# Kernel optimization log

Measured on AMD Instinct MI355X. Metric: run time of the kernel, lower is better.

## Reference

```python
import jax, jax.numpy as jnp
import numpy as np

N = 4096
IN_DIM = 6
HID = 32
HEADS1 = 4
OUT_DIM = 64


def _gat_layer(x, mask, W, a_src, a_dst, b):
    # x: [n, in], W: [in, heads*d], a_src/a_dst: [heads, d], b: [heads*d]
    n = x.shape[0]
    heads, d = a_src.shape
    h = (x @ W).reshape(n, heads, d)                      # [n, heads, d]
    e_src = jnp.einsum('nhd,hd->nh', h, a_src)            # [n, heads]
    e_dst = jnp.einsum('nhd,hd->nh', h, a_dst)            # [n, heads]
    logits = e_src[:, None, :] + e_dst[None, :, :]        # [n, n, heads]
    logits = jax.nn.leaky_relu(logits, negative_slope=0.2)
    logits = jnp.where(mask[:, :, None], logits, jnp.float32(-1e9))
    alpha = jax.nn.softmax(logits, axis=1)                # softmax over j (dim=1)
    # dropout disabled (eval mode reference)
    out = jnp.einsum('ijh,jhd->ihd', alpha, h).reshape(n, heads * d)
    return out + b


def setup_inputs() -> dict:
    key = jax.random.key(0)
    ks = jax.random.split(key, 10)
    x = jax.random.normal(ks[0], (N, IN_DIM), dtype=jnp.float32)
    adj = jax.random.bernoulli(ks[1], 0.01, (N, N)).astype(jnp.float32)
    s = 0.1
    W1 = jax.random.normal(ks[2], (IN_DIM, HEADS1 * HID), dtype=jnp.float32) * s
    a_src1 = jax.random.normal(ks[3], (HEADS1, HID), dtype=jnp.float32) * s
    a_dst1 = jax.random.normal(ks[4], (HEADS1, HID), dtype=jnp.float32) * s
    b1 = jnp.zeros((HEADS1 * HID,), dtype=jnp.float32)
    W2 = jax.random.normal(ks[5], (HEADS1 * HID, OUT_DIM), dtype=jnp.float32) * s
    a_src2 = jax.random.normal(ks[6], (1, OUT_DIM), dtype=jnp.float32) * s
    a_dst2 = jax.random.normal(ks[7], (1, OUT_DIM), dtype=jnp.float32) * s
    b2 = jnp.zeros((OUT_DIM,), dtype=jnp.float32)
    return {'x': x, 'adj': adj, 'W1': W1, 'a_src1': a_src1, 'a_dst1': a_dst1,
            'b1': b1, 'W2': W2, 'a_src2': a_src2, 'a_dst2': a_dst2, 'b2': b2}


def reference(x, adj, W1, a_src1, a_dst1, b1, W2, a_src2, a_dst2, b2):
    n = x.shape[0]
    # add self loops: a = max(a, I), mask = a > 0
    a = jnp.maximum(adj, jnp.eye(n, dtype=adj.dtype))
    mask = a > 0
    h1 = jax.nn.elu(_gat_layer(x, mask, W1, a_src1, a_dst1, b1))
    # dropout disabled (eval mode)
    h2 = _gat_layer(h1, mask, W2, a_src2, a_dst2, b2)
    return h2
```

## Files before the change

kernel.cpp:

```cpp
#include <hip/hip_runtime.h>

#define N 4096
#define IN_DIM 6
#define HID 32
#define HEADS1 4
#define D1 (HEADS1*HID)
#define OUT_DIM 64
#define MAXNB 192

__global__ void kA(const float* __restrict__ x,
                   const float* __restrict__ W1,
                   const float* __restrict__ a_src1,
                   const float* __restrict__ a_dst1,
                   float* __restrict__ hpre,
                   float* __restrict__ es1,
                   float* __restrict__ ed1) {
    int t  = threadIdx.x;
    int r  = t >> 7;
    int tt = t & 127;
    int i  = blockIdx.x * 2 + r;
    __shared__ float xs[2][IN_DIM];
    if (tt < IN_DIM) xs[r][tt] = x[i*IN_DIM + tt];
    __syncthreads();
    float acc = 0.f;
    #pragma unroll
    for (int k = 0; k < IN_DIM; ++k)
        acc += xs[r][k] * W1[k*D1 + tt];
    hpre[(size_t)i*D1 + tt] = acc;
    float ps = acc * a_src1[tt];
    float pd = acc * a_dst1[tt];
    #pragma unroll
    for (int off = 16; off >= 1; off >>= 1) {
        ps += __shfl_xor(ps, off, 64);
        pd += __shfl_xor(pd, off, 64);
    }
    if ((tt & 31) == 0) {
        int h = tt >> 5;
        es1[i*HEADS1 + h] = ps;
        ed1[i*HEADS1 + h] = pd;
    }
}

__global__ void kB(const float* __restrict__ adj,
                   const float* __restrict__ hpre,
                   const float* __restrict__ es1,
                   const float* __restrict__ ed1,
                   const float* __restrict__ b1,
                   const float* __restrict__ W2,
                   const float* __restrict__ a_src2,
                   const float* __restrict__ a_dst2,
                   int* __restrict__ cnt, int* __restrict__ idxg,
                   float* __restrict__ h2pre,
                   float* __restrict__ es2, float* __restrict__ ed2) {
    int i = blockIdx.x;
    int t = threadIdx.x;
    __shared__ int   cL;
    __shared__ int   js[MAXNB];
    __shared__ float lg[HEADS1][MAXNB];
    __shared__ float esi[HEADS1];
    __shared__ float sinv[HEADS1];
    __shared__ float part[128];
    __shared__ float h1s[D1];
    __shared__ float p2s[256];
    if (t == 0) cL = 0;
    if (t < HEADS1) esi[t] = es1[i*HEADS1 + t];
    __syncthreads();

    const float4* row  = (const float4*)(adj + (size_t)i * N);
    const float4* ed1v = (const float4*)ed1;
    for (int k = t; k < N/4; k += 256) {
        float4 v = row[k];
        float f[4] = {v.x, v.y, v.z, v.w};
        #pragma unroll
        for (int q = 0; q < 4; ++q) {
            int j = k*4 + q;
            if (f[q] > 0.f || j == i) {
                int p = atomicAdd(&cL, 1);
                if (p < MAXNB) {
                    js[p] = j;
                    float4 e4 = ed1v[j];
                    float le[4] = {e4.x, e4.y, e4.z, e4.w};
                    #pragma unroll
                    for (int h = 0; h < HEADS1; ++h) {
                        float l = esi[h] + le[h];
                        lg[h][p] = (l > 0.f) ? l : 0.2f*l;
                    }
                }
            }
        }
    }
    __syncthreads();
    int c = min(cL, MAXNB);

    if (t >= 128) {
        if (t == 128) cnt[i] = c;
        for (int p = t - 128; p < c; p += 128) idxg[i*MAXNB + p] = js[p];
    } else {
        int h = t >> 5, lane = t & 31;
        float m = -1e30f;
        for (int p = lane; p < c; p += 32) m = fmaxf(m, lg[h][p]);
        #pragma unroll
        for (int off = 16; off >= 1; off >>= 1) m = fmaxf(m, __shfl_xor(m, off, 64));
        float s = 0.f;
        for (int p = lane; p < c; p += 32) {
            float e = __expf(lg[h][p] - m);
            lg[h][p] = e;
            s += e;
        }
        #pragma unroll
        for (int off = 16; off >= 1; off >>= 1) s += __shfl_xor(s, off, 64);
        if (lane == 0) sinv[h] = 1.f / s;
    }
    __syncthreads();

    int g = t >> 7, tt = t & 127, hh = (t & 127) >> 5;
    float acc = 0.f;
    for (int p = g; p < c; p += 2)
        acc += lg[hh][p] * hpre[(size_t)js[p]*D1 + tt];
    if (g == 1) part[tt] = acc;
    __syncthreads();
    if (g == 0) {
        acc += part[tt];
        float val = acc * sinv[hh] + b1[tt];
        h1s[tt] = (val > 0.f) ? val : expm1f(val);
    }
    __syncthreads();

    int o = t & 63, q = t >> 6;
    float pa = 0.f;
    #pragma unroll
    for (int k = 0; k < 32; ++k) {
        int kk = q*32 + k;
        pa += h1s[kk] * W2[kk*OUT_DIM + o];
    }
    p2s[t] = pa;
    __syncthreads();
    if (t < 64) {
        float h2 = p2s[t] + p2s[t+64] + p2s[t+128] + p2s[t+192];
        h2pre[(size_t)i*OUT_DIM + t] = h2;
        float ps = h2 * a_src2[t];
        float pd = h2 * a_dst2[t];
        #pragma unroll
        for (int off = 32; off >= 1; off >>= 1) {
            ps += __shfl_xor(ps, off, 64);
            pd += __shfl_xor(pd, off, 64);
        }
        if (t == 0) { es2[i] = ps; ed2[i] = pd; }
    }
}

__global__ void kC(const float* __restrict__ h2pre,
                   const float* __restrict__ es2,
                   const float* __restrict__ ed2,
                   const int* __restrict__ cnt,
                   const int* __restrict__ idxg,
                   const float* __restrict__ b2v,
                   float* __restrict__ out) {
    int i = blockIdx.x;
    int t = threadIdx.x;
    int c = cnt[i];
    __shared__ int   js[MAXNB];
    __shared__ float al[MAXNB];
    for (int p = t; p < c; p += 64) js[p] = idxg[i*MAXNB + p];
    __syncthreads();
    float esi = es2[i];
    float m = -1e30f;
    for (int p = t; p < c; p += 64) {
        float l = esi + ed2[js[p]];
        l = (l > 0.f) ? l : 0.2f*l;
        al[p] = l;
        m = fmaxf(m, l);
    }
    #pragma unroll
    for (int off = 32; off >= 1; off >>= 1) m = fmaxf(m, __shfl_xor(m, off, 64));
    __syncthreads();
    float s = 0.f;
    for (int p = t; p < c; p += 64) {
        float e = __expf(al[p] - m);
        al[p] = e;
        s += e;
    }
    #pragma unroll
    for (int off = 32; off >= 1; off >>= 1) s += __shfl_xor(s, off, 64);
    float inv = 1.f / s;
    __syncthreads();
    float acc = 0.f;
    for (int p = 0; p < c; ++p)
        acc += al[p] * h2pre[(size_t)js[p]*OUT_DIM + t];
    out[(size_t)i*OUT_DIM + t] = acc * inv + b2v[t];
}

extern "C" void kernel_launch(void* const* d_in, const int* in_sizes, int n_in,
                              void* d_out, int out_size, void* d_ws, size_t ws_size,
                              hipStream_t stream) {
    const float* x      = (const float*)d_in[0];
    const float* adj    = (const float*)d_in[1];
    const float* W1     = (const float*)d_in[2];
    const float* a_src1 = (const float*)d_in[3];
    const float* a_dst1 = (const float*)d_in[4];
    const float* b1     = (const float*)d_in[5];
    const float* W2     = (const float*)d_in[6];
    const float* a_src2 = (const float*)d_in[7];
    const float* a_dst2 = (const float*)d_in[8];
    const float* b2v    = (const float*)d_in[9];
    float* out = (float*)d_out;

    float* ws    = (float*)d_ws;
    float* hpre  = ws;
    float* h2pre = hpre  + (size_t)N*D1;
    float* es1   = h2pre + (size_t)N*OUT_DIM;
    float* ed1   = es1   + (size_t)N*HEADS1;
    float* es2   = ed1   + (size_t)N*HEADS1;
    float* ed2   = es2   + N;
    int*   cnt   = (int*)(ed2 + N);
    int*   idxg  = cnt + N;

    kA<<<N/2, 256, 0, stream>>>(x, W1, a_src1, a_dst1, hpre, es1, ed1);
    kB<<<N,   256, 0, stream>>>(adj, hpre, es1, ed1, b1, W2, a_src2, a_dst2,
                                cnt, idxg, h2pre, es2, ed2);
    kC<<<N,    64, 0, stream>>>(h2pre, es2, ed2, cnt, idxg, b2v, out);
}
```

Baseline: 148.6 us.

## Widen GAT row blocks and split neighbor aggregation across more threads

New measurement: 137.1 us. 1.08x faster.

```diff
diff --git a/kernel.cpp b/kernel.cpp
--- a/kernel.cpp
+++ b/kernel.cpp
@@ -41,7 +41,8 @@
     }
 }
 
-__global__ void kB(const float* __restrict__ adj,
+__global__ __launch_bounds__(512) void kB(
+                   const float* __restrict__ adj,
                    const float* __restrict__ hpre,
                    const float* __restrict__ es1,
                    const float* __restrict__ ed1,
@@ -59,68 +60,81 @@
     __shared__ float lg[HEADS1][MAXNB];
     __shared__ float esi[HEADS1];
     __shared__ float sinv[HEADS1];
-    __shared__ float part[128];
+    __shared__ float part[3][D1];
     __shared__ float h1s[D1];
-    __shared__ float p2s[256];
+    __shared__ float p2s[512];
     if (t == 0) cL = 0;
     if (t < HEADS1) esi[t] = es1[i*HEADS1 + t];
     __syncthreads();
 
-    const float4* row  = (const float4*)(adj + (size_t)i * N);
-    const float4* ed1v = (const float4*)ed1;
-    for (int k = t; k < N/4; k += 256) {
-        float4 v = row[k];
-        float f[4] = {v.x, v.y, v.z, v.w};
-        #pragma unroll
-        for (int q = 0; q < 4; ++q) {
-            int j = k*4 + q;
-            if (f[q] > 0.f || j == i) {
-                int p = atomicAdd(&cL, 1);
-                if (p < MAXNB) {
-                    js[p] = j;
-                    float4 e4 = ed1v[j];
-                    float le[4] = {e4.x, e4.y, e4.z, e4.w};
-                    #pragma unroll
-                    for (int h = 0; h < HEADS1; ++h) {
-                        float l = esi[h] + le[h];
-                        lg[h][p] = (l > 0.f) ? l : 0.2f*l;
-                    }
-                }
-            }
+    const float4* row = (const float4*)(adj + (size_t)i * N);
+    float4 v0 = row[t];
+    float4 v1 = row[t + 512];
+    float f[8] = {v0.x, v0.y, v0.z, v0.w, v1.x, v1.y, v1.z, v1.w};
+    #pragma unroll
+    for (int q = 0; q < 8; ++q) {
+        int j = (q < 4) ? (t*4 + q) : (2048 + t*4 + (q - 4));
+        if (f[q] > 0.f || j == i) {
+            int p = atomicAdd(&cL, 1);
+            if (p < MAXNB) js[p] = j;
         }
     }
     __syncthreads();
     int c = min(cL, MAXNB);
 
-    if (t >= 128) {
-        if (t == 128) cnt[i] = c;
-        for (int p = t - 128; p < c; p += 128) idxg[i*MAXNB + p] = js[p];
-    } else {
-        int h = t >> 5, lane = t & 31;
+    if (t < c) {
+        int j = js[t];
+        float4 e4 = ((const float4*)ed1)[j];
+        float l0 = esi[0] + e4.x, l1 = esi[1] + e4.y,
+              l2 = esi[2] + e4.z, l3 = esi[3] + e4.w;
+        lg[0][t] = (l0 > 0.f) ? l0 : 0.2f*l0;
+        lg[1][t] = (l1 > 0.f) ? l1 : 0.2f*l1;
+        lg[2][t] = (l2 > 0.f) ? l2 : 0.2f*l2;
+        lg[3][t] = (l3 > 0.f) ? l3 : 0.2f*l3;
+    }
+    if (t >= 256) {
+        int p = t - 256;
+        if (p == 0) cnt[i] = c;
+        if (p < c) idxg[i*MAXNB + p] = js[p];
+    }
+    __syncthreads();
+
+    if (t < 256) {
+        int h = t >> 6, l = t & 63;
         float m = -1e30f;
-        for (int p = lane; p < c; p += 32) m = fmaxf(m, lg[h][p]);
-        #pragma unroll
-        for (int off = 16; off >= 1; off >>= 1) m = fmaxf(m, __shfl_xor(m, off, 64));
+        for (int p = l; p < c; p += 64) m = fmaxf(m, lg[h][p]);
+        #pragma unroll
+        for (int off = 32; off >= 1; off >>= 1) m = fmaxf(m, __shfl_xor(m, off, 64));
         float s = 0.f;
-        for (int p = lane; p < c; p += 32) {
+        for (int p = l; p < c; p += 64) {
             float e = __expf(lg[h][p] - m);
             lg[h][p] = e;
             s += e;
         }
         #pragma unroll
-        for (int off = 16; off >= 1; off >>= 1) s += __shfl_xor(s, off, 64);
-        if (lane == 0) sinv[h] = 1.f / s;
-    }
-    __syncthreads();
-
-    int g = t >> 7, tt = t & 127, hh = (t & 127) >> 5;
+        for (int off = 32; off >= 1; off >>= 1) s += __shfl_xor(s, off, 64);
+        if (l == 0) sinv[h] = 1.f / s;
+    }
+    __syncthreads();
+
+    int g = t >> 7, tt = t & 127, hh = tt >> 5;
     float acc = 0.f;
-    for (int p = g; p < c; p += 2)
+    int p = g;
+    for (; p + 12 < c; p += 16) {
+        int   j0 = js[p],      j1 = js[p+4],   j2 = js[p+8],   j3 = js[p+12];
+        float w0 = lg[hh][p],  w1 = lg[hh][p+4], w2 = lg[hh][p+8], w3 = lg[hh][p+12];
+        float x0 = hpre[(size_t)j0*D1 + tt];
+        float x1 = hpre[(size_t)j1*D1 + tt];
+        float x2 = hpre[(size_t)j2*D1 + tt];
+        float x3 = hpre[(size_t)j3*D1 + tt];
+        acc += w0*x0 + w1*x1 + w2*x2 + w3*x3;
+    }
+    for (; p < c; p += 4)
         acc += lg[hh][p] * hpre[(size_t)js[p]*D1 + tt];
-    if (g == 1) part[tt] = acc;
+    if (g) part[g-1][tt] = acc;
     __syncthreads();
     if (g == 0) {
-        acc += part[tt];
+        acc += part[0][tt] + part[1][tt] + part[2][tt];
         float val = acc * sinv[hh] + b1[tt];
         h1s[tt] = (val > 0.f) ? val : expm1f(val);
     }
@@ -129,14 +143,16 @@
     int o = t & 63, q = t >> 6;
     float pa = 0.f;
     #pragma unroll
-    for (int k = 0; k < 32; ++k) {
-        int kk = q*32 + k;
+    for (int k = 0; k < 16; ++k) {
+        int kk = q*16 + k;
         pa += h1s[kk] * W2[kk*OUT_DIM + o];
     }
     p2s[t] = pa;
     __syncthreads();
     if (t < 64) {
-        float h2 = p2s[t] + p2s[t+64] + p2s[t+128] + p2s[t+192];
+        float h2 = 0.f;
+        #pragma unroll
+        for (int qq = 0; qq < 8; ++qq) h2 += p2s[t + 64*qq];
         h2pre[(size_t)i*OUT_DIM + t] = h2;
         float ps = h2 * a_src2[t];
         float pd = h2 * a_dst2[t];
@@ -149,7 +165,8 @@
     }
 }
 
-__global__ void kC(const float* __restrict__ h2pre,
+__global__ __launch_bounds__(256) void kC(
+                   const float* __restrict__ h2pre,
                    const float* __restrict__ es2,
                    const float* __restrict__ ed2,
                    const int* __restrict__ cnt,
@@ -161,33 +178,52 @@
     int c = cnt[i];
     __shared__ int   js[MAXNB];
     __shared__ float al[MAXNB];
-    for (int p = t; p < c; p += 64) js[p] = idxg[i*MAXNB + p];
-    __syncthreads();
+    __shared__ float sinv_s;
+    __shared__ float part[3][OUT_DIM];
     float esi = es2[i];
-    float m = -1e30f;
-    for (int p = t; p < c; p += 64) {
-        float l = esi + ed2[js[p]];
-        l = (l > 0.f) ? l : 0.2f*l;
-        al[p] = l;
-        m = fmaxf(m, l);
-    }
-    #pragma unroll
-    for (int off = 32; off >= 1; off >>= 1) m = fmaxf(m, __shfl_xor(m, off, 64));
-    __syncthreads();
-    float s = 0.f;
-    for (int p = t; p < c; p += 64) {
-        float e = __expf(al[p] - m);
-        al[p] = e;
-        s += e;
-    }
-    #pragma unroll
-    for (int off = 32; off >= 1; off >>= 1) s += __shfl_xor(s, off, 64);
-    float inv = 1.f / s;
-    __syncthreads();
+    if (t < c) {
+        int j = idxg[i*MAXNB + t];
+        js[t] = j;
+        float l = esi + ed2[j];
+        al[t] = (l > 0.f) ? l : 0.2f*l;
+    }
+    __syncthreads();
+    if (t < 64) {
+        float m = -1e30f;
+        for (int p = t; p < c; p += 64) m = fmaxf(m, al[p]);
+        #pragma unroll
+        for (int off = 32; off >= 1; off >>= 1) m = fmaxf(m, __shfl_xor(m, off, 64));
+        float s = 0.f;
+        for (int p = t; p < c; p += 64) {
+            float e = __expf(al[p] - m);
+            al[p] = e;
+            s += e;
+        }
+        #pragma unroll
+        for (int off = 32; off >= 1; off >>= 1) s += __shfl_xor(s, off, 64);
+        if (t == 0) sinv_s = 1.f / s;
+    }
+    __syncthreads();
+    int g = t >> 6, o = t & 63;
     float acc = 0.f;
-    for (int p = 0; p < c; ++p)
-        acc += al[p] * h2pre[(size_t)js[p]*OUT_DIM + t];
-    out[(size_t)i*OUT_DIM + t] = acc * inv + b2v[t];
+    int p = g;
+    for (; p + 12 < c; p += 16) {
+        int   j0 = js[p],    j1 = js[p+4],  j2 = js[p+8],  j3 = js[p+12];
+        float w0 = al[p],    w1 = al[p+4],  w2 = al[p+8],  w3 = al[p+12];
+        float x0 = h2pre[(size_t)j0*OUT_DIM + o];
+        float x1 = h2pre[(size_t)j1*OUT_DIM + o];
+        float x2 = h2pre[(size_t)j2*OUT_DIM + o];
+        float x3 = h2pre[(size_t)j3*OUT_DIM + o];
+        acc += w0*x0 + w1*x1 + w2*x2 + w3*x3;
+    }
+    for (; p < c; p += 4)
+        acc += al[p] * h2pre[(size_t)js[p]*OUT_DIM + o];
+    if (g) part[g-1][o] = acc;
+    __syncthreads();
+    if (g == 0) {
+        acc += part[0][o] + part[1][o] + part[2][o];
+        out[(size_t)i*OUT_DIM + o] = acc * sinv_s + b2v[o];
+    }
 }
 
 extern "C" void kernel_launch(void* const* d_in, const int* in_sizes, int n_in,
@@ -216,7 +252,7 @@
     int*   idxg  = cnt + N;
 
     kA<<<N/2, 256, 0, stream>>>(x, W1, a_src1, a_dst1, hpre, es1, ed1);
-    kB<<<N,   256, 0, stream>>>(adj, hpre, es1, ed1, b1, W2, a_src2, a_dst2,
+    kB<<<N,   512, 0, stream>>>(adj, hpre, es1, ed1, b1, W2, a_src2, a_dst2,
                                 cnt, idxg, h2pre, es2, ed2);
-    kC<<<N,    64, 0, stream>>>(h2pre, es2, ed2, cnt, idxg, b2v, out);
-}
+    kC<<<N,   256, 0, stream>>>(h2pre, es2, ed2, cnt, idxg, b2v, out);
+}
```
